# Optimization experiments

Measured on AMD Instinct MI355X. Metric: run time of the kernel, lower is better.

## Reference

```python
import jax, jax.numpy as jnp
import numpy as np

STRONG = 255.0
WEAK = 25.0
HIGH_T = 0.15
LOW_T = 0.05


def setup_inputs() -> dict:
    key = jax.random.key(0)
    img = jax.random.uniform(key, (1, 1, 2048, 2048), dtype=jnp.float32)
    return {"img": img}


def _shl(v):  # neighbor at j+1
    return jnp.concatenate([v[1:], jnp.zeros((1,), dtype=bool)])


def _shr(v):  # neighbor at j-1
    return jnp.concatenate([jnp.zeros((1,), dtype=bool), v[:-1]])


def reference(img):
    x = img[0, 0]  # (H, W)
    H, W = x.shape
    high = x.max() * HIGH_T
    low = high * LOW_T  # note: low = high * low_threshold, per the torch source
    # Double threshold. In the torch code strong is assigned first, then weak
    # overwrites pixels with img == high, so the tie goes to WEAK:
    t = jnp.where(x < low, 0.0, jnp.where(x <= high, WEAK, STRONG))

    cols = jnp.arange(W)
    col_interior = (cols >= 1) & (cols <= W - 2)

    def combine(l, r):
        # linear boolean recurrence x[j] = a[j] | (b[j] & x[j-1])
        al, bl = l
        ar, br = r
        return (ar | (br & al), bl & br)

    def row_step(prev_new, rows):
        cur, nxt = rows
        ps = prev_new == STRONG   # row above: already updated (raster order)
        cs = cur == STRONG        # current row: original (right neighbor not yet updated)
        ns = nxt == STRONG        # row below: original
        # strong among the 7 non-left neighbors
        base = _shr(ps) | ps | _shl(ps) | _shl(cs) | _shr(ns) | ns | _shl(ns)
        weak = (cur == WEAK) & col_interior
        a = cs | (weak & base)
        b = weak
        strong_flag, _ = jax.lax.associative_scan(combine, (a, b))
        new = jnp.where(weak, jnp.where(strong_flag, STRONG, 0.0), cur)
        return new, new

    _, inner = jax.lax.scan(row_step, t[0], (t[1:-1], t[2:]))
    out = jnp.concatenate([t[:1], inner, t[-1:]], axis=0)
    return out[None, None]
```

## Files before the change

kernel.cpp:

```cpp
#include <hip/hip_runtime.h>

#define IMG_H 2048
#define IMG_W 2048
#define RSTRIPE 8
#define NSTRIPES 256
#define MAXBLOCKS 1024
#define MAGIC 0x5ca1ab1eu

typedef unsigned long long ull;

__device__ __forceinline__ unsigned interior_mask(int lane) {
    unsigned m = 0xffffffffu;
    if (lane == 0)  m &= ~1u;
    if (lane == 63) m &= 0x7fffffffu;
    return m;
}

struct RowCtx {
    unsigned b1, b2, b4, b8, b16, lowrun, a_static;
    ull B1, B2, B4, B8, B16, B32;
};

__device__ __forceinline__ RowCtx make_ctx(unsigned cs, ull cs_lsb,
                                           unsigned ns, ull ns_lsb, ull ns_msb,
                                           unsigned wk, unsigned interior, int lane) {
    RowCtx c;
    c.b1 = wk & interior;
    unsigned rcs = (cs >> 1) | (((unsigned)((cs_lsb >> 1 >> lane) & 1ull)) << 31);
    unsigned rns = (ns >> 1) | (((unsigned)((ns_lsb >> 1 >> lane) & 1ull)) << 31);
    unsigned lns = (ns << 1) | ((unsigned)(((ns_msb << 1) >> lane) & 1ull));
    c.a_static = cs | (c.b1 & (rcs | lns | ns | rns));
    c.b2  = c.b1 & (c.b1 << 1);
    c.b4  = c.b2 & (c.b2 << 2);
    c.b8  = c.b4 & (c.b4 << 4);
    c.b16 = c.b8 & (c.b8 << 8);
    c.lowrun = c.b1 & (c.b1 ^ (c.b1 + 1u));
    c.B1  = __ballot(c.b1 == 0xffffffffu);
    c.B2  = c.B1  & (c.B1  << 1);
    c.B4  = c.B2  & (c.B2  << 2);
    c.B8  = c.B4  & (c.B4  << 4);
    c.B16 = c.B8  & (c.B8  << 8);
    c.B32 = c.B16 & (c.B16 << 16);
    return c;
}

__device__ __forceinline__ unsigned rowstep(unsigned ps, const RowCtx& c, int lane) {
    ull ps_msb = __ballot(ps >> 31);
    ull ps_lsb = __ballot(ps & 1u);
    unsigned lps = (ps << 1) | ((unsigned)(((ps_msb << 1) >> lane) & 1ull));
    unsigned rps = (ps >> 1) | (((unsigned)((ps_lsb >> 1 >> lane) & 1ull)) << 31);
    unsigned x = c.a_static | (c.b1 & (lps | ps | rps));
    x |= c.b1  & (x << 1);
    x |= c.b2  & (x << 2);
    x |= c.b4  & (x << 4);
    x |= c.b8  & (x << 8);
    x |= c.b16 & (x << 16);
    ull X = __ballot(x >> 31);
    X |= c.B1  & (X << 1);
    X |= c.B2  & (X << 2);
    X |= c.B4  & (X << 4);
    X |= c.B8  & (X << 8);
    X |= c.B16 & (X << 16);
    X |= c.B32 & (X << 32);
    unsigned carry = (unsigned)(((X << 1) >> lane) & 1ull);
    x |= carry ? c.lowrun : 0u;
    return x;
}

__device__ __forceinline__ void binrow(const float* __restrict__ img, int r, int lane,
                                       float high, float low,
                                       unsigned* sOut, unsigned* wOut) {
    const float4* p = (const float4*)(img + r * IMG_W + lane * 32);
    unsigned sb = 0, tb = 0;
#pragma unroll
    for (int i = 0; i < 8; ++i) {
        float4 v = p[i];
        sb |= (v.x > high ? 1u : 0u) << (4 * i);
        sb |= (v.y > high ? 1u : 0u) << (4 * i + 1);
        sb |= (v.z > high ? 1u : 0u) << (4 * i + 2);
        sb |= (v.w > high ? 1u : 0u) << (4 * i + 3);
        tb |= (v.x >= low ? 1u : 0u) << (4 * i);
        tb |= (v.y >= low ? 1u : 0u) << (4 * i + 1);
        tb |= (v.z >= low ? 1u : 0u) << (4 * i + 2);
        tb |= (v.w >= low ? 1u : 0u) << (4 * i + 3);
    }
    *sOut = sb;
    *wOut = tb & ~sb;
}

__global__ __launch_bounds__(256) void max_part_kernel(const float4* __restrict__ in,
                                                       float* __restrict__ partial) {
    __shared__ float sm[4];
    int base = blockIdx.x * 1024 + threadIdx.x;
    float m = 0.0f;
#pragma unroll
    for (int i = 0; i < 4; ++i) {
        float4 v = in[base + i * 256];
        m = fmaxf(fmaxf(m, v.x), fmaxf(v.y, fmaxf(v.z, v.w)));
    }
#pragma unroll
    for (int off = 32; off > 0; off >>= 1)
        m = fmaxf(m, __shfl_down(m, off, 64));
    if ((threadIdx.x & 63) == 0) sm[threadIdx.x >> 6] = m;
    __syncthreads();
    if (threadIdx.x == 0)
        partial[blockIdx.x] = fmaxf(fmaxf(sm[0], sm[1]), fmaxf(sm[2], sm[3]));
}

__global__ __launch_bounds__(256) void mega_kernel(const float* __restrict__ img,
                                                   const float* __restrict__ partial,
                                                   float* __restrict__ out,
                                                   unsigned* __restrict__ Nlast,
                                                   unsigned* __restrict__ done) {
    __shared__ unsigned ldsS[10][64], ldsW[10][64], ldsX[RSTRIPE][64];
    __shared__ float sm[4];
    const int t = threadIdx.x, wave = t >> 6, lane = t & 63;
    const int s = blockIdx.x;
    const int start = 1 + RSTRIPE * s;
    const int nown = min(start + RSTRIPE, 2047) - start;

    float m = fmaxf(fmaxf(partial[t], partial[t + 256]),
                    fmaxf(partial[t + 512], partial[t + 768]));
#pragma unroll
    for (int off = 32; off > 0; off >>= 1)
        m = fmaxf(m, __shfl_down(m, off, 64));
    if (lane == 0) sm[wave] = m;
    __syncthreads();
    const float maxv = fmaxf(fmaxf(sm[0], sm[1]), fmaxf(sm[2], sm[3]));
    const float high = maxv * 0.15f;
    const float low  = high * 0.05f;

    for (int u = wave; u < 10; u += 4) {
        int r = min(start - 1 + u, 2047);
        unsigned sb, wb;
        binrow(img, r, lane, high, low, &sb, &wb);
        ldsS[u][lane] = sb;
        ldsW[u][lane] = wb;
    }
    __syncthreads();

    if (wave == 0) {
        const unsigned interior = interior_mask(lane);
        unsigned pcs = ldsS[0][lane], pw = ldsW[0][lane];
        unsigned psl = pcs;
        unsigned psu = (s == 0) ? pcs : (pcs | (pw & interior));
        unsigned cs = ldsS[1][lane];
        ull cs_lsb = __ballot(cs & 1u);
        int conv_u = nown;
        bool converged = false;
#pragma unroll
        for (int u = 0; u < RSTRIPE; ++u) {
            if (u < nown) {
                unsigned ns = ldsS[u + 2][lane];
                unsigned wk = ldsW[u + 1][lane];
                ull ns_lsb = __ballot(ns & 1u);
                ull ns_msb = __ballot(ns >> 31);
                RowCtx c = make_ctx(cs, cs_lsb, ns, ns_lsb, ns_msb, wk, interior, lane);
                unsigned xu = rowstep(psu, c, lane);
                unsigned xl;
                if (!converged) {
                    xl = rowstep(psl, c, lane);
                    if (__ballot(xl != xu) == 0ull) { converged = true; conv_u = u; }
                } else {
                    xl = xu;
                }
                ldsX[u][lane] = xu;
                psl = xl;
                psu = xu;
                cs = ns;
                cs_lsb = ns_lsb;
            }
        }
        if (s > 0 && conv_u > 0) {
            if (lane == 0) {
                while (atomicOr(&done[s - 1], 0u) != MAGIC) {}
            }
            __threadfence();
            unsigned ps = Nlast[(s - 1) * 64 + lane];
            unsigned cs2 = ldsS[1][lane];
            ull cs2_lsb = __ballot(cs2 & 1u);
            for (int u = 0; u < conv_u; ++u) {
                unsigned ns = ldsS[u + 2][lane];
                unsigned wk = ldsW[u + 1][lane];
                ull ns_lsb = __ballot(ns & 1u);
                ull ns_msb = __ballot(ns >> 31);
                RowCtx c = make_ctx(cs2, cs2_lsb, ns, ns_lsb, ns_msb, wk, interior, lane);
                unsigned x = rowstep(ps, c, lane);
                ldsX[u][lane] = x;
                ps = x;
                cs2 = ns;
                cs2_lsb = ns_lsb;
            }
        }
        if (s < NSTRIPES - 1) {
            Nlast[s * 64 + lane] = ldsX[RSTRIPE - 1][lane];
            __threadfence();
            if (lane == 0) atomicExch(&done[s], MAGIC);
        }
    }
    __syncthreads();

    for (int u = wave; u < nown; u += 4) {
        int r = start + u;
        unsigned x = ldsX[u][lane];
        unsigned w = ldsW[u + 1][lane];
        float4* po = (float4*)(out + r * IMG_W + lane * 32);
#pragma unroll
        for (int i = 0; i < 8; ++i) {
            float4 o;
            float* f = (float*)&o;
#pragma unroll
            for (int k2 = 0; k2 < 4; ++k2) {
                int k = 4 * i + k2;
                bool sn = (x >> k) & 1u;
                bool wb = (w >> k) & 1u;
                bool ec = (lane == 0 && k == 0) || (lane == 63 && k == 31);
                f[k2] = sn ? 255.0f : ((wb && ec) ? 25.0f : 0.0f);
            }
            po[i] = o;
        }
    }
    if ((s == 0 && wave == 1) || (s == NSTRIPES - 1 && wave == 2)) {
        int u = (s == 0) ? 0 : 7;
        int r = (s == 0) ? 0 : 2047;
        unsigned sw = ldsS[u][lane];
        unsigned ww = ldsW[u][lane];
        float4* po = (float4*)(out + r * IMG_W + lane * 32);
#pragma unroll
        for (int i = 0; i < 8; ++i) {
            float4 o;
            float* f = (float*)&o;
#pragma unroll
            for (int k2 = 0; k2 < 4; ++k2) {
                int k = 4 * i + k2;
                bool sn = (sw >> k) & 1u;
                bool wb = (ww >> k) & 1u;
                f[k2] = sn ? 255.0f : (wb ? 25.0f : 0.0f);
            }
            po[i] = o;
        }
    }
}

extern "C" void kernel_launch(void* const* d_in, const int* in_sizes, int n_in,
                              void* d_out, int out_size, void* d_ws, size_t ws_size,
                              hipStream_t stream) {
    const float* img = (const float*)d_in[0];
    char* ws = (char*)d_ws;
    float* partial = (float*)(ws);
    unsigned* done  = (unsigned*)(ws + 8192);
    unsigned* Nlast = (unsigned*)(ws + 16384);

    max_part_kernel<<<MAXBLOCKS, 256, 0, stream>>>((const float4*)img, partial);
    mega_kernel<<<NSTRIPES, 256, 0, stream>>>(img, partial, (float*)d_out, Nlast, done);
}
```

Baseline: 83.15 us.

## Split float expansion out of chained stripe kernel into separate bitmask expand pass

The stripe kernel now writes only packed strong and edge-weak bitmasks to workspace instead of expanding to floats in-kernel. A new fully parallel kernel then expands those bitmasks into the 16 MB float output. The aim is to shorten the serialized, chained stripe kernel so the expensive output write no longer sits inside the inter-block dependency chain. The cost is an extra launch plus a small bitmask round-trip through global memory.

```diff
diff --git a/kernel.cpp b/kernel.cpp
--- a/kernel.cpp
+++ b/kernel.cpp
@@ -107,12 +107,13 @@
         partial[blockIdx.x] = fmaxf(fmaxf(sm[0], sm[1]), fmaxf(sm[2], sm[3]));
 }
 
-__global__ __launch_bounds__(256) void mega_kernel(const float* __restrict__ img,
-                                                   const float* __restrict__ partial,
-                                                   float* __restrict__ out,
-                                                   unsigned* __restrict__ Nlast,
-                                                   unsigned* __restrict__ done) {
-    __shared__ unsigned ldsS[10][64], ldsW[10][64], ldsX[RSTRIPE][64];
+__global__ __launch_bounds__(256) void spec2_kernel(const float* __restrict__ img,
+                                                    const float* __restrict__ partial,
+                                                    unsigned* __restrict__ outS,
+                                                    unsigned* __restrict__ outW25,
+                                                    unsigned* __restrict__ Nlast,
+                                                    unsigned* __restrict__ done) {
+    __shared__ unsigned ldsS[10][64], ldsW[10][64];
     __shared__ float sm[4];
     const int t = threadIdx.x, wave = t >> 6, lane = t & 63;
     const int s = blockIdx.x;
@@ -139,6 +140,8 @@
     }
     __syncthreads();
 
+    const unsigned emask = (lane == 0 ? 1u : 0u) | (lane == 63 ? 0x80000000u : 0u);
+
     if (wave == 0) {
         const unsigned interior = interior_mask(lane);
         unsigned pcs = ldsS[0][lane], pw = ldsW[0][lane];
@@ -146,6 +149,7 @@
         unsigned psu = (s == 0) ? pcs : (pcs | (pw & interior));
         unsigned cs = ldsS[1][lane];
         ull cs_lsb = __ballot(cs & 1u);
+        unsigned xbuf[RSTRIPE];
         int conv_u = nown;
         bool converged = false;
 #pragma unroll
@@ -164,7 +168,8 @@
                 } else {
                     xl = xu;
                 }
-                ldsX[u][lane] = xu;
+                xbuf[u] = xu;
+                outW25[(start + u) * 64 + lane] = wk & emask;
                 psl = xl;
                 psu = xu;
                 cs = ns;
@@ -186,60 +191,45 @@
                 ull ns_msb = __ballot(ns >> 31);
                 RowCtx c = make_ctx(cs2, cs2_lsb, ns, ns_lsb, ns_msb, wk, interior, lane);
                 unsigned x = rowstep(ps, c, lane);
-                ldsX[u][lane] = x;
+                xbuf[u] = x;
                 ps = x;
                 cs2 = ns;
                 cs2_lsb = ns_lsb;
             }
         }
+#pragma unroll
+        for (int u = 0; u < RSTRIPE; ++u)
+            if (u < nown) outS[(start + u) * 64 + lane] = xbuf[u];
         if (s < NSTRIPES - 1) {
-            Nlast[s * 64 + lane] = ldsX[RSTRIPE - 1][lane];
+            Nlast[s * 64 + lane] = xbuf[RSTRIPE - 1];
             __threadfence();
             if (lane == 0) atomicExch(&done[s], MAGIC);
         }
     }
-    __syncthreads();
-
-    for (int u = wave; u < nown; u += 4) {
-        int r = start + u;
-        unsigned x = ldsX[u][lane];
-        unsigned w = ldsW[u + 1][lane];
-        float4* po = (float4*)(out + r * IMG_W + lane * 32);
-#pragma unroll
-        for (int i = 0; i < 8; ++i) {
-            float4 o;
-            float* f = (float*)&o;
-#pragma unroll
-            for (int k2 = 0; k2 < 4; ++k2) {
-                int k = 4 * i + k2;
-                bool sn = (x >> k) & 1u;
-                bool wb = (w >> k) & 1u;
-                bool ec = (lane == 0 && k == 0) || (lane == 63 && k == 31);
-                f[k2] = sn ? 255.0f : ((wb && ec) ? 25.0f : 0.0f);
-            }
-            po[i] = o;
-        }
-    }
     if ((s == 0 && wave == 1) || (s == NSTRIPES - 1 && wave == 2)) {
         int u = (s == 0) ? 0 : 7;
         int r = (s == 0) ? 0 : 2047;
-        unsigned sw = ldsS[u][lane];
-        unsigned ww = ldsW[u][lane];
-        float4* po = (float4*)(out + r * IMG_W + lane * 32);
-#pragma unroll
-        for (int i = 0; i < 8; ++i) {
-            float4 o;
-            float* f = (float*)&o;
-#pragma unroll
-            for (int k2 = 0; k2 < 4; ++k2) {
-                int k = 4 * i + k2;
-                bool sn = (sw >> k) & 1u;
-                bool wb = (ww >> k) & 1u;
-                f[k2] = sn ? 255.0f : (wb ? 25.0f : 0.0f);
-            }
-            po[i] = o;
-        }
-    }
+        outS[r * 64 + lane]   = ldsS[u][lane];
+        outW25[r * 64 + lane] = ldsW[u][lane];
+    }
+}
+
+__global__ __launch_bounds__(256) void expand2_kernel(const unsigned* __restrict__ outS,
+                                                      const unsigned* __restrict__ outW25,
+                                                      float4* __restrict__ out) {
+    int tid = blockIdx.x * blockDim.x + threadIdx.x;
+    int p = tid << 2;
+    unsigned sb = outS[p >> 5];
+    unsigned wb = outW25[p >> 5];
+    int bit = p & 31;
+    float4 o;
+    float* f = (float*)&o;
+#pragma unroll
+    for (int k = 0; k < 4; ++k) {
+        int b = bit + k;
+        f[k] = ((sb >> b) & 1u) ? 255.0f : (((wb >> b) & 1u) ? 25.0f : 0.0f);
+    }
+    out[tid] = o;
 }
 
 extern "C" void kernel_launch(void* const* d_in, const int* in_sizes, int n_in,
@@ -247,10 +237,13 @@
                               hipStream_t stream) {
     const float* img = (const float*)d_in[0];
     char* ws = (char*)d_ws;
-    float* partial = (float*)(ws);
-    unsigned* done  = (unsigned*)(ws + 8192);
-    unsigned* Nlast = (unsigned*)(ws + 16384);
+    float* partial   = (float*)ws;
+    unsigned* done   = (unsigned*)(ws + 8192);
+    unsigned* Nlast  = (unsigned*)(ws + 16384);
+    unsigned* outS   = (unsigned*)(ws + (1 << 17));
+    unsigned* outW25 = (unsigned*)(ws + (1 << 17) + (1 << 19));
 
     max_part_kernel<<<MAXBLOCKS, 256, 0, stream>>>((const float4*)img, partial);
-    mega_kernel<<<NSTRIPES, 256, 0, stream>>>(img, partial, (float*)d_out, Nlast, done);
-}
+    spec2_kernel<<<NSTRIPES, 256, 0, stream>>>(img, partial, outS, outW25, Nlast, done);
+    expand2_kernel<<<(IMG_H * IMG_W / 4) / 256, 256, 0, stream>>>(outS, outW25, (float4*)d_out);
+}
```

Measured after the change: 83.82 us. Within noise of the previous version (+0.8%).
